# Performance work log

Hardware: AMD Instinct MI355X
Metric: run time of the kernel (lower is better)

## Reference

```python
import jax, jax.numpy as jnp
import numpy as np

HEAD_DIM = 128  # dim // num_heads; RoPE rot_dim and softmax scale
ROPE_THETA = 10000.0


def rope_rotate(x, rot_dim):
    # lucidrains RotaryEmbedding.rotate_queries_or_keys: rotate first rot_dim
    # channels of last axis with interleaved-pair rotation; pass rest through.
    T = x.shape[-2]
    inv_freq = 1.0 / (ROPE_THETA ** (jnp.arange(0, rot_dim, 2, dtype=jnp.float32) / rot_dim))
    freqs = jnp.arange(T, dtype=jnp.float32)[:, None] * inv_freq[None, :]  # [T, rot_dim//2]
    freqs = jnp.repeat(freqs, 2, axis=-1)  # [T, rot_dim] interleaved (f0,f0,f1,f1,...)
    cos, sin = jnp.cos(freqs), jnp.sin(freqs)
    xr, x_pass = x[..., :rot_dim], x[..., rot_dim:]
    x1, x2 = xr[..., 0::2], xr[..., 1::2]
    rot = jnp.stack([-x2, x1], axis=-1).reshape(xr.shape)  # rotate_half
    xr = xr * cos + rot * sin
    return jnp.concatenate([xr, x_pass], axis=-1)


def setup_inputs() -> dict:
    key = jax.random.key(0)
    ks = jax.random.split(key, 9)
    B, T, D = 2, 2048, 2048
    w = lambda k, shape: jax.random.normal(k, shape, dtype=jnp.float32) * 0.02
    return {
        "latent_space": jax.random.normal(ks[0], (B, T, D), dtype=jnp.float32),
        "Wq": w(ks[1], (D, D)), "bq": w(ks[2], (D,)),
        "Wk": w(ks[3], (D, D)), "bk": w(ks[4], (D,)),
        "Wv": w(ks[5], (D, D)), "bv": w(ks[6], (D,)),
        "Wfc": w(ks[7], (D, D)), "bfc": w(ks[8], (D,)),
    }


def reference(latent_space, Wq, bq, Wk, bk, Wv, bv, Wfc, bfc):
    # Projections (nn.Linear: x @ W.T + b)
    Q = latent_space @ Wq.T + bq
    K = latent_space @ Wk.T + bk
    V = latent_space @ Wv.T + bv
    # Fused RoPE on first HEAD_DIM channels (module never splits heads)
    Q = rope_rotate(Q, HEAD_DIM)
    K = rope_rotate(K, HEAD_DIM)
    # Full-hidden-dim QK^T: [B,T,T]
    qk = jnp.einsum('btd,bsd->bts', Q, K)
    T = qk.shape[-1]
    causal = jnp.triu(jnp.ones((T, T), dtype=bool), 1)
    A = jnp.where(causal, -jnp.inf, qk)
    # PartialSoftmax with temp=1, h_t=None: state = A/sqrt(head_dim);
    # out = exp(state)/sum(exp(state)) * 2
    state = A / jnp.sqrt(jnp.float32(HEAD_DIM))
    x_exp = jnp.exp(state)
    A = x_exp / jnp.sum(x_exp, axis=-1, keepdims=True) * 2.0
    out = jnp.einsum('bts,bsd->btd', A, V) @ Wfc.T + bfc
    return out
```

## Files before the change

kernel.cpp:

```cpp
#include <hip/hip_runtime.h>
#include <hip/hip_bf16.h>
#include <math.h>

using bf16 = __hip_bfloat16;
typedef __attribute__((ext_vector_type(8))) __bf16 bf16x8;
typedef __attribute__((ext_vector_type(4))) float f32x4;

#define SBAR() asm volatile("s_barrier" ::: "memory")
#define WAITVM(n) asm volatile("s_waitcnt vmcnt(" #n ")" ::: "memory")

static __device__ __forceinline__ void gload16(const bf16* g, bf16* l) {
  __builtin_amdgcn_global_load_lds((const __attribute__((address_space(1))) void*)g,
                                   (__attribute__((address_space(3))) void*)l, 16, 0, 0);
}

struct GP {
  const bf16* A[6]; const bf16* B[6]; char* C[6];
  const float* bias[6];
  int K[6], flags[6], ktOff[6];
};
struct CvtP { const float* s[5]; bf16* d[5]; int n4[5]; };

__global__ __launch_bounds__(256) void cvt_f32_bf16(CvtP p) {
  const int y = blockIdx.y;
  const int i = blockIdx.x * 256 + threadIdx.x;
  if (i >= p.n4[y]) return;
  const float4 v = reinterpret_cast<const float4*>(p.s[y])[i];
  union { bf16 h[4]; short4 s4; } u;
  u.h[0] = __float2bfloat16(v.x);
  u.h[1] = __float2bfloat16(v.y);
  u.h[2] = __float2bfloat16(v.z);
  u.h[3] = __float2bfloat16(v.w);
  *reinterpret_cast<short4*>(p.d[y] + 4 * (size_t)i) = u.s4;
}

__global__ __launch_bounds__(512, 1) void gemm8(GP P, int lda, int ldb, int ldc) {
  const int z = blockIdx.z;
  const int fl = P.flags[z];
  if ((fl & 1) && blockIdx.x > blockIdx.y) return;
  const int by = (fl & 8) ? ((int)gridDim.y - 1 - (int)blockIdx.y) : (int)blockIdx.y;
  const int rowBase = by * 256;
  const int colBase = (int)blockIdx.x * 256;
  int kEnd = P.K[z];
  if (fl & 8) {
    const int lim = rowBase + 256 - P.ktOff[z];
    kEnd = kEnd < lim ? kEnd : lim;
    if (kEnd <= 0) return;
  }
  const int NT = kEnd >> 5;

  const int tid  = threadIdx.x;
  const int lane = tid & 63;
  const int wid  = tid >> 6;
  const int wm = wid >> 2;
  const int wn = wid & 3;

  __shared__ alignas(16) bf16 ls[4][16384];

  f32x4 acc[8][4] = {};

  const int rt  = tid >> 2;
  const int sw8 = ((tid & 3) ^ ((rt >> 1) & 3)) * 8;
  const bf16* gA0 = P.A[z] + (size_t)(rowBase + rt) * lda + sw8;
  const bf16* gA1 = gA0 + (size_t)128 * lda;
  const bf16* gB0 = P.B[z] + (size_t)(colBase + rt) * ldb + sw8;
  const bf16* gB1 = gB0 + (size_t)128 * ldb;

  const int lr = lane >> 4, lc = lane & 15;
  const int kb = (lr ^ ((lc >> 1) & 3)) * 8;

#define STAGE(t) { bf16* d = &ls[(t) & 3][0]; const int ko = (t) * 32; \
    gload16(gA0 + ko, &d[tid * 8]); \
    gload16(gA1 + ko, &d[4096 + tid * 8]); \
    gload16(gB0 + ko, &d[8192 + tid * 8]); \
    gload16(gB1 + ko, &d[12288 + tid * 8]); }

  STAGE(0); STAGE(1); STAGE(2);

  for (int t = 0; t < NT; ++t) {
    if (t < NT - 2)       WAITVM(8);
    else if (t == NT - 2) WAITVM(4);
    else                  WAITVM(0);
    SBAR();
    const bf16* LA = &ls[t & 3][0];
    const bf16* LB = &ls[t & 3][8192];
    bf16x8 af[8], bfr[4];
#pragma unroll
    for (int m = 0; m < 8; ++m)
      af[m] = *reinterpret_cast<const bf16x8*>(&LA[(wm * 128 + m * 16 + lc) * 32 + kb]);
#pragma unroll
    for (int n = 0; n < 4; ++n)
      bfr[n] = *reinterpret_cast<const bf16x8*>(&LB[(wn * 64 + n * 16 + lc) * 32 + kb]);
    if (t + 3 < NT) STAGE(t + 3);
    SBAR();
    __builtin_amdgcn_s_setprio(1);
#pragma unroll
    for (int m = 0; m < 8; ++m)
#pragma unroll
      for (int n = 0; n < 4; ++n)
        acc[m][n] = __builtin_amdgcn_mfma_f32_16x16x32_bf16(af[m], bfr[n], acc[m][n], 0, 0, 0);
    __builtin_amdgcn_s_setprio(0);
  }
#undef STAGE

  const float* bias = P.bias[z];
  char* C = P.C[z];
#pragma unroll
  for (int m = 0; m < 8; ++m) {
    const int row0 = rowBase + wm * 128 + m * 16 + lr * 4;
#pragma unroll
    for (int n = 0; n < 4; ++n) {
      const int col = colBase + wn * 64 + n * 16 + lc;
      const float bcol = (bias && !(fl & 2)) ? bias[col] : 0.f;
#pragma unroll
      for (int j = 0; j < 4; ++j) {
        float v = acc[m][n][j] + bcol;
        if (fl & 2) v += bias[row0 + j];
        const long idx = (long)(row0 + j) * ldc + col;
        if (fl & 4) reinterpret_cast<float*>(C)[idx] = v;
        else        reinterpret_cast<bf16*>(C)[idx] = __float2bfloat16(v);
      }
    }
  }
}

__global__ __launch_bounds__(256) void rope_bf16(bf16* __restrict__ X) {
  const int idx = blockIdx.x * 256 + threadIdx.x;
  const int row = idx >> 6;
  const int i   = idx & 63;
  const int t   = row & 2047;
  const float ang = (float)t * exp2f((float)i * -0.20762050593046f);
  float sn, cs;
  sincosf(ang, &sn, &cs);
  bf16* p = X + ((long)row << 11) + 2 * i;
  const float x1 = __bfloat162float(p[0]);
  const float x2 = __bfloat162float(p[1]);
  p[0] = __float2bfloat16(x1 * cs - x2 * sn);
  p[1] = __float2bfloat16(x2 * cs + x1 * sn);
}

__global__ __launch_bounds__(256) void softmax_causal(
    const float* __restrict__ S0, const float* __restrict__ S1,
    const float* __restrict__ S2, const float* __restrict__ S3,
    bf16* __restrict__ A0, bf16* __restrict__ A1) {
  const int t = blockIdx.x;
  const int b = blockIdx.y;
  const float* ra = (b ? S2 : S0) + (long)t * 2048;
  const float* rb = (b ? S3 : S1) + (long)t * 2048;
  bf16* orow = (b ? A1 : A0) + (long)t * 4096;
  const int L = t + 1;
  __shared__ float e[2048];
  __shared__ float red[4];
  const float scale = 0.0883883476483184f;
  const int lane = threadIdx.x & 63, wd = threadIdx.x >> 6;

  float mx = -INFINITY;
  for (int s = threadIdx.x; s < L; s += 256) {
    const float v = (ra[s] + rb[s]) * scale;
    e[s] = v;
    mx = fmaxf(mx, v);
  }
#pragma unroll
  for (int off = 1; off < 64; off <<= 1) mx = fmaxf(mx, __shfl_xor(mx, off));
  if (lane == 0) red[wd] = mx;
  __syncthreads();
  mx = fmaxf(fmaxf(red[0], red[1]), fmaxf(red[2], red[3]));
  __syncthreads();

  float sum = 0.f;
  for (int s = threadIdx.x; s < L; s += 256) {
    const float v = expf(e[s] - mx);
    e[s] = v;
    sum += v;
  }
#pragma unroll
  for (int off = 1; off < 64; off <<= 1) sum += __shfl_xor(sum, off);
  if (lane == 0) red[wd] = sum;
  __syncthreads();
  sum = red[0] + red[1] + red[2] + red[3];
  const float f = 2.f / sum;
  for (int s = threadIdx.x; s < 2048; s += 256) {
    const float v = (s < L) ? e[s] * f : 0.f;
    orow[s] = __float2bfloat16(v);
  }
}

__global__ __launch_bounds__(256) void pv_reduce(
    const float* __restrict__ p0a, const float* __restrict__ p0b,
    const float* __restrict__ p1, bf16* __restrict__ O) {
  const long i4 = (long)blockIdx.x * 256 + threadIdx.x;
  const long g = i4 * 4;
  const int b = (int)(g >> 22);
  const long rem = g & ((1L << 22) - 1);
  const int r = (int)(rem >> 11);
  const float* p0 = b ? p0b : p0a;
  float4 v = *reinterpret_cast<const float4*>(p0 + rem);
  if (r >= 1024) {
    const float4 w = *reinterpret_cast<const float4*>(
        p1 + (long)b * (1024 * 2048) + (rem - (1L << 21)));
    v.x += w.x; v.y += w.y; v.z += w.z; v.w += w.w;
  }
  union { bf16 h[4]; short4 s; } u;
  u.h[0] = __float2bfloat16(v.x);
  u.h[1] = __float2bfloat16(v.y);
  u.h[2] = __float2bfloat16(v.z);
  u.h[3] = __float2bfloat16(v.w);
  *reinterpret_cast<short4*>(O + g) = u.s;
}

__global__ __launch_bounds__(256) void fc_reduce(
    const float* __restrict__ pa, const float* __restrict__ pb,
    const float* __restrict__ bias, float* __restrict__ out) {
  const long i4 = (long)blockIdx.x * 256 + threadIdx.x;
  const long g = i4 * 4;
  const int col = (int)(g & 2047);
  const float4 a = reinterpret_cast<const float4*>(pa)[i4];
  const float4 b4 = reinterpret_cast<const float4*>(pb)[i4];
  const float4 bv = *reinterpret_cast<const float4*>(bias + col);
  float4 o;
  o.x = a.x + b4.x + bv.x;
  o.y = a.y + b4.y + bv.y;
  o.z = a.z + b4.z + bv.z;
  o.w = a.w + b4.w + bv.w;
  reinterpret_cast<float4*>(out)[i4] = o;
}

extern "C" void kernel_launch(void* const* d_in, const int* in_sizes, int n_in,
                              void* d_out, int out_size, void* d_ws, size_t ws_size,
                              hipStream_t stream) {
  (void)in_sizes; (void)n_in; (void)out_size; (void)ws_size;
  const float* lat = (const float*)d_in[0];
  const float* Wq  = (const float*)d_in[1];
  const float* bq  = (const float*)d_in[2];
  const float* Wk  = (const float*)d_in[3];
  const float* bk  = (const float*)d_in[4];
  const float* Wv  = (const float*)d_in[5];
  const float* bv  = (const float*)d_in[6];
  const float* Wfc = (const float*)d_in[7];
  const float* bfc = (const float*)d_in[8];
  float* out = (float*)d_out;

  constexpr long T = 2048, D = 2048, MT = 4096;
  constexpr long TTB = T * T * 4;
  char* w = (char*)d_ws;
  bf16* latb = (bf16*)w;  w += MT * D * 2;
  bf16* wqb  = (bf16*)w;  w += D * D * 2;
  bf16* wkb  = (bf16*)w;  w += D * D * 2;
  bf16* wvb  = (bf16*)w;  w += D * D * 2;
  bf16* wfb  = (bf16*)w;  w += D * D * 2;
  bf16* Qb   = (bf16*)w;  w += MT * D * 2;
  bf16* Kb   = (bf16*)w;  w += MT * D * 2;
  bf16* VTb  = (bf16*)w;  w += MT * D * 2;
  float* S0  = (float*)w; w += TTB;
  float* S1  = (float*)w; w += TTB;
  float* P1w = (float*)w; w += TTB;
  float* S2  = (float*)d_out;
  float* S3  = (float*)((char*)d_out + TTB);
  bf16* A0   = (bf16*)S0;
  bf16* A1   = (bf16*)S3;
  float* P0a = S1;
  float* P0b = S2;
  bf16* Ob   = latb;
  float* Pf0 = (float*)Qb;
  float* Pf1 = S0;

  CvtP cp;
  cp.s[0] = lat; cp.d[0] = latb; cp.n4[0] = (int)(MT * D / 4);
  cp.s[1] = Wq;  cp.d[1] = wqb;  cp.n4[1] = (int)(D * D / 4);
  cp.s[2] = Wk;  cp.d[2] = wkb;  cp.n4[2] = (int)(D * D / 4);
  cp.s[3] = Wv;  cp.d[3] = wvb;  cp.n4[3] = (int)(D * D / 4);
  cp.s[4] = Wfc; cp.d[4] = wfb;  cp.n4[4] = (int)(D * D / 4);
  cvt_f32_bf16<<<dim3(8192, 5), 256, 0, stream>>>(cp);

  {
    GP P = {};
    P.A[0] = latb; P.B[0] = wqb; P.C[0] = (char*)Qb; P.bias[0] = bq; P.K[0] = 2048;
    P.A[1] = latb; P.B[1] = wkb; P.C[1] = (char*)Kb; P.bias[1] = bk; P.K[1] = 2048;
    gemm8<<<dim3(8, 16, 2), 512, 0, stream>>>(P, 2048, 2048, 2048);
  }

  rope_bf16<<<2048, 256, 0, stream>>>(Qb);

  {
    GP P = {};
    for (int b = 0; b < 2; ++b) {
      P.A[b] = wvb; P.B[b] = latb + (long)b * T * D;
      P.C[b] = (char*)(VTb + (long)b * T * D);
      P.bias[b] = bv; P.K[b] = 2048; P.flags[b] = 2;
    }
    char* sc[4] = {(char*)S0, (char*)S1, (char*)S2, (char*)S3};
    for (int zz = 0; zz < 4; ++zz) {
      const int b = zz >> 1, kh = zz & 1;
      P.A[2 + zz] = Qb + (long)b * T * D + kh * 1024;
      P.B[2 + zz] = Kb + (long)b * T * D + kh * 1024;
      P.C[2 + zz] = sc[zz];
      P.K[2 + zz] = 1024; P.flags[2 + zz] = 1 | 4;
    }
    gemm8<<<dim3(8, 8, 6), 512, 0, stream>>>(P, 2048, 2048, 2048);
  }

  softmax_causal<<<dim3(2048, 2), 256, 0, stream>>>(S0, S1, S2, S3, A0, A1);

  {
    GP P = {};
    for (int z = 0; z < 4; ++z) {
      const int b = z >> 1, kh = z & 1;
      P.A[z] = (b ? A1 : A0) + kh * 1024;
      P.B[z] = VTb + (long)b * T * D + kh * 1024;
      P.C[z] = kh ? ((char*)P1w + (long)b * 1024 * 2048 * 4 - (long)1024 * 2048 * 4)
                  : (char*)(b ? P0b : P0a);
      P.K[z] = 1024; P.flags[z] = 8 | 4; P.ktOff[z] = kh * 1024;
    }
    gemm8<<<dim3(8, 8, 4), 512, 0, stream>>>(P, 4096, 2048, 2048);
  }

  pv_reduce<<<8192, 256, 0, stream>>>(P0a, P0b, P1w, Ob);

  {
    GP P = {};
    for (int kh = 0; kh < 2; ++kh) {
      P.A[kh] = Ob + kh * 1024;
      P.B[kh] = wfb + kh * 1024;
      P.C[kh] = (char*)(kh ? Pf1 : Pf0);
      P.K[kh] = 1024; P.flags[kh] = 4;
    }
    gemm8<<<dim3(8, 16, 2), 512, 0, stream>>>(P, 2048, 2048, 2048);
  }

  fc_reduce<<<8192, 256, 0, stream>>>(Pf0, Pf1, bfc, out);
}
```

Measured before the change: 303.2 us.

## Restructure GEMM main loop into 64-wide K steps with four-phase ping-pong pipeline

The GEMM kernel now processes K in steps of 64 using a double-buffered LDS layout split into four 128-row quarters. Each step runs four compute phases, and the global-to-LDS load for the next step's matching quarter is issued inside each phase. The aim is to interleave LDS fragment reads, async global loads and MFMA work more finely and to hide load latency. In exchange it adds more barriers per iteration and needs K to be a multiple of 64, which the causal-trimmed kEnd may not always be.

```diff
diff --git a/kernel.cpp b/kernel.cpp
--- a/kernel.cpp
+++ b/kernel.cpp
@@ -8,6 +8,7 @@
 
 #define SBAR() asm volatile("s_barrier" ::: "memory")
 #define WAITVM(n) asm volatile("s_waitcnt vmcnt(" #n ")" ::: "memory")
+#define LGKM0() { asm volatile("s_waitcnt lgkmcnt(0)" ::: "memory"); __builtin_amdgcn_sched_barrier(0); }
 
 static __device__ __forceinline__ void gload16(const bf16* g, bf16* l) {
   __builtin_amdgcn_global_load_lds((const __attribute__((address_space(1))) void*)g,
@@ -34,7 +35,7 @@
   *reinterpret_cast<short4*>(p.d[y] + 4 * (size_t)i) = u.s4;
 }
 
-__global__ __launch_bounds__(512, 1) void gemm8(GP P, int lda, int ldb, int ldc) {
+__global__ __launch_bounds__(512, 1) void gemm8p(GP P, int lda, int ldb, int ldc) {
   const int z = blockIdx.z;
   const int fl = P.flags[z];
   if ((fl & 1) && blockIdx.x > blockIdx.y) return;
@@ -47,7 +48,7 @@
     kEnd = kEnd < lim ? kEnd : lim;
     if (kEnd <= 0) return;
   }
-  const int NT = kEnd >> 5;
+  const int NT = kEnd >> 6;
 
   const int tid  = threadIdx.x;
   const int lane = tid & 63;
@@ -55,53 +56,111 @@
   const int wm = wid >> 2;
   const int wn = wid & 3;
 
-  __shared__ alignas(16) bf16 ls[4][16384];
+  __shared__ alignas(16) bf16 ls[2][4][8192];
 
   f32x4 acc[8][4] = {};
 
-  const int rt  = tid >> 2;
-  const int sw8 = ((tid & 3) ^ ((rt >> 1) & 3)) * 8;
-  const bf16* gA0 = P.A[z] + (size_t)(rowBase + rt) * lda + sw8;
-  const bf16* gA1 = gA0 + (size_t)128 * lda;
-  const bf16* gB0 = P.B[z] + (size_t)(colBase + rt) * ldb + sw8;
-  const bf16* gB1 = gB0 + (size_t)128 * ldb;
+  const int r0  = tid >> 2;
+  const int sw8 = ((tid & 3) ^ ((r0 >> 1) & 3)) * 8;
+  const bf16* gA = P.A[z] + (size_t)(rowBase + r0) * lda + sw8;
+  const bf16* gB = P.B[z] + (size_t)(colBase + r0) * ldb + sw8;
 
   const int lr = lane >> 4, lc = lane & 15;
-  const int kb = (lr ^ ((lc >> 1) & 3)) * 8;
-
-#define STAGE(t) { bf16* d = &ls[(t) & 3][0]; const int ko = (t) * 32; \
-    gload16(gA0 + ko, &d[tid * 8]); \
-    gload16(gA1 + ko, &d[4096 + tid * 8]); \
-    gload16(gB0 + ko, &d[8192 + tid * 8]); \
-    gload16(gB1 + ko, &d[12288 + tid * 8]); }
-
-  STAGE(0); STAGE(1); STAGE(2);
+  int aoff[8], boff[4];
+#pragma unroll
+  for (int mi = 0; mi < 8; ++mi) {
+    const int row = wm * 128 + mi * 16 + lc;
+    aoff[mi] = row * 32 + (lr ^ ((row >> 1) & 3)) * 8;
+  }
+#pragma unroll
+  for (int ni = 0; ni < 4; ++ni) {
+    const int row = wn * 64 + ni * 16 + lc;
+    boff[ni] = row * 32 + (lr ^ ((row >> 1) & 3)) * 8;
+  }
+
+#define STG(t, h) { bf16* d = &ls[(t) & 1][h][0]; \
+    if ((h) < 2) { const int ko = (t) * 64 + (h) * 32; \
+      gload16(gA + ko, &d[tid * 8]); \
+      gload16(gA + (size_t)128 * lda + ko, &d[4096 + tid * 8]); \
+    } else { const int ko = (t) * 64 + ((h) - 2) * 32; \
+      gload16(gB + ko, &d[tid * 8]); \
+      gload16(gB + (size_t)128 * ldb + ko, &d[4096 + tid * 8]); } }
+
+  STG(0, 0); STG(0, 2); STG(0, 1); STG(0, 3);
+  WAITVM(0);
+  SBAR();
 
   for (int t = 0; t < NT; ++t) {
-    if (t < NT - 2)       WAITVM(8);
-    else if (t == NT - 2) WAITVM(4);
-    else                  WAITVM(0);
-    SBAR();
-    const bf16* LA = &ls[t & 3][0];
-    const bf16* LB = &ls[t & 3][8192];
-    bf16x8 af[8], bfr[4];
-#pragma unroll
-    for (int m = 0; m < 8; ++m)
-      af[m] = *reinterpret_cast<const bf16x8*>(&LA[(wm * 128 + m * 16 + lc) * 32 + kb]);
-#pragma unroll
-    for (int n = 0; n < 4; ++n)
-      bfr[n] = *reinterpret_cast<const bf16x8*>(&LB[(wn * 64 + n * 16 + lc) * 32 + kb]);
-    if (t + 3 < NT) STAGE(t + 3);
-    SBAR();
+    const bf16* LA0 = &ls[t & 1][0][0];
+    const bf16* LA1 = &ls[t & 1][1][0];
+    const bf16* LB0 = &ls[t & 1][2][0];
+    const bf16* LB1 = &ls[t & 1][3][0];
+    const bool more = (t + 1 < NT);
+    bf16x8 a0[4], a1[4], b0[4], b1[4];
+
+#pragma unroll
+    for (int i = 0; i < 4; ++i) a0[i] = *(const bf16x8*)&LA0[aoff[i]];
+#pragma unroll
+    for (int i = 0; i < 4; ++i) b0[i] = *(const bf16x8*)&LB0[boff[i]];
+    if (more) STG(t + 1, 0);
+    SBAR();
+    LGKM0();
     __builtin_amdgcn_s_setprio(1);
 #pragma unroll
-    for (int m = 0; m < 8; ++m)
+    for (int m = 0; m < 4; ++m)
 #pragma unroll
       for (int n = 0; n < 4; ++n)
-        acc[m][n] = __builtin_amdgcn_mfma_f32_16x16x32_bf16(af[m], bfr[n], acc[m][n], 0, 0, 0);
+        acc[m][n] = __builtin_amdgcn_mfma_f32_16x16x32_bf16(a0[m], b0[n], acc[m][n], 0, 0, 0);
     __builtin_amdgcn_s_setprio(0);
-  }
-#undef STAGE
+    SBAR();
+
+#pragma unroll
+    for (int i = 0; i < 4; ++i) a1[i] = *(const bf16x8*)&LA0[aoff[4 + i]];
+    if (more) STG(t + 1, 2);
+    if (t + 1 == NT) { WAITVM(0); } else { WAITVM(4); }
+    SBAR();
+    LGKM0();
+    __builtin_amdgcn_s_setprio(1);
+#pragma unroll
+    for (int m = 0; m < 4; ++m)
+#pragma unroll
+      for (int n = 0; n < 4; ++n)
+        acc[4 + m][n] = __builtin_amdgcn_mfma_f32_16x16x32_bf16(a1[m], b0[n], acc[4 + m][n], 0, 0, 0);
+    __builtin_amdgcn_s_setprio(0);
+    SBAR();
+
+#pragma unroll
+    for (int i = 0; i < 4; ++i) a0[i] = *(const bf16x8*)&LA1[aoff[i]];
+#pragma unroll
+    for (int i = 0; i < 4; ++i) b1[i] = *(const bf16x8*)&LB1[boff[i]];
+    if (more) STG(t + 1, 1);
+    SBAR();
+    LGKM0();
+    __builtin_amdgcn_s_setprio(1);
+#pragma unroll
+    for (int m = 0; m < 4; ++m)
+#pragma unroll
+      for (int n = 0; n < 4; ++n)
+        acc[m][n] = __builtin_amdgcn_mfma_f32_16x16x32_bf16(a0[m], b1[n], acc[m][n], 0, 0, 0);
+    __builtin_amdgcn_s_setprio(0);
+    SBAR();
+
+#pragma unroll
+    for (int i = 0; i < 4; ++i) a1[i] = *(const bf16x8*)&LA1[aoff[4 + i]];
+    if (more) STG(t + 1, 3);
+    WAITVM(4);
+    SBAR();
+    LGKM0();
+    __builtin_amdgcn_s_setprio(1);
+#pragma unroll
+    for (int m = 0; m < 4; ++m)
+#pragma unroll
+      for (int n = 0; n < 4; ++n)
+        acc[4 + m][n] = __builtin_amdgcn_mfma_f32_16x16x32_bf16(a1[m], b1[n], acc[4 + m][n], 0, 0, 0);
+    __builtin_amdgcn_s_setprio(0);
+    SBAR();
+  }
+#undef STG
 
   const float* bias = P.bias[z];
   char* C = P.C[z];
@@ -276,7 +335,7 @@
     GP P = {};
     P.A[0] = latb; P.B[0] = wqb; P.C[0] = (char*)Qb; P.bias[0] = bq; P.K[0] = 2048;
     P.A[1] = latb; P.B[1] = wkb; P.C[1] = (char*)Kb; P.bias[1] = bk; P.K[1] = 2048;
-    gemm8<<<dim3(8, 16, 2), 512, 0, stream>>>(P, 2048, 2048, 2048);
+    gemm8p<<<dim3(8, 16, 2), 512, 0, stream>>>(P, 2048, 2048, 2048);
   }
 
   rope_bf16<<<2048, 256, 0, stream>>>(Qb);
@@ -296,7 +355,7 @@
       P.C[2 + zz] = sc[zz];
       P.K[2 + zz] = 1024; P.flags[2 + zz] = 1 | 4;
     }
-    gemm8<<<dim3(8, 8, 6), 512, 0, stream>>>(P, 2048, 2048, 2048);
+    gemm8p<<<dim3(8, 8, 6), 512, 0, stream>>>(P, 2048, 2048, 2048);
   }
 
   softmax_causal<<<dim3(2048, 2), 256, 0, stream>>>(S0, S1, S2, S3, A0, A1);
@@ -311,7 +370,7 @@
                   : (char*)(b ? P0b : P0a);
       P.K[z] = 1024; P.flags[z] = 8 | 4; P.ktOff[z] = kh * 1024;
     }
-    gemm8<<<dim3(8, 8, 4), 512, 0, stream>>>(P, 4096, 2048, 2048);
+    gemm8p<<<dim3(8, 8, 4), 512, 0, stream>>>(P, 4096, 2048, 2048);
   }
 
   pv_reduce<<<8192, 256, 0, stream>>>(P0a, P0b, P1w, Ob);
@@ -324,7 +383,7 @@
       P.C[kh] = (char*)(kh ? Pf1 : Pf0);
       P.K[kh] = 1024; P.flags[kh] = 4;
     }
-    gemm8<<<dim3(8, 16, 2), 512, 0, stream>>>(P, 2048, 2048, 2048);
+    gemm8p<<<dim3(8, 16, 2), 512, 0, stream>>>(P, 2048, 2048, 2048);
   }
 
   fc_reduce<<<8192, 256, 0, stream>>>(Pf0, Pf1, bfc, out);
```

After: 303.8 us. No clear change (+0.2%).
